# Kernel optimization log

Measured on AMD Instinct MI355X. Metric: run time of the kernel, lower is better.

## Reference

```python
import jax, jax.numpy as jnp
import numpy as np

H = 8          # head_num
NEG = -1e9     # mask fill value
LN_EPS = 1e-6


def setup_inputs() -> dict:
    key = jax.random.key(0)
    ks = jax.random.split(key, 12)
    B, S, D = 8, 1024, 512
    inp = {
        'q': jax.random.normal(ks[0], (B, S, D), jnp.float32),
        'k': jax.random.normal(ks[1], (B, S, D), jnp.float32),
        'v': jax.random.normal(ks[2], (B, S, D), jnp.float32),
        'query_mask': jax.random.randint(ks[3], (B, S), 0, 2, jnp.int32),
        'key_mask': jax.random.randint(ks[4], (B, S), 0, 2, jnp.int32),
        'Wq': jax.random.normal(ks[5], (D, D), jnp.float32) / np.sqrt(D),
        'bq': jax.random.normal(ks[6], (D,), jnp.float32) * 0.02,
        'Wk': jax.random.normal(ks[7], (D, D), jnp.float32) / np.sqrt(D),
        'bk': jax.random.normal(ks[8], (D,), jnp.float32) * 0.02,
        'Wv': jax.random.normal(ks[9], (D, D), jnp.float32) / np.sqrt(D),
        'bv': jax.random.normal(ks[10], (D,), jnp.float32) * 0.02,
        'gamma': jnp.ones((D,), jnp.float32),
        'beta': jnp.zeros((D,), jnp.float32),
    }
    return inp


def _to_batches(x):
    # [B,S,D] -> [B*H, S, D/H]  (batch-major head layout, as in torch code)
    B, S, D = x.shape
    return x.reshape(B, S, H, D // H).transpose(0, 2, 1, 3).reshape(B * H, S, D // H)


def _from_batches(x):
    BH, S, d = x.shape
    B = BH // H
    return x.reshape(B, H, S, d).transpose(0, 2, 1, 3).reshape(B, S, H * d)


def reference(q, k, v, query_mask, key_mask, Wq, bq, Wk, bk, Wv, bv, gamma, beta):
    # QKV linears + ReLU activation (activation=F.relu in original)
    _q = jax.nn.relu(q @ Wq.T + bq)
    _k = jax.nn.relu(k @ Wk.T + bk)
    _v = jax.nn.relu(v @ Wv.T + bv)
    _q, _k, _v = _to_batches(_q), _to_batches(_k), _to_batches(_v)  # [B*H,S,d]

    # masks tiled head-MAJOR (repeat(head_num,1) semantics): index = h*B + b
    km = jnp.tile(key_mask, (H, 1))[:, None, :]    # [B*H, 1, S_k]
    qm = jnp.tile(query_mask, (H, 1))[:, :, None]  # [B*H, S_q, 1]

    d = _q.shape[-1]
    scores = jnp.einsum('bqd,bkd->bqk', _q, _k) / jnp.sqrt(jnp.float32(d))
    scores = jnp.where(km == 0, NEG, scores)
    attn = jax.nn.softmax(scores, axis=-1)
    attn = attn * qm.astype(attn.dtype)            # multiplicative query mask
    # dropout: eval mode (rate applied only in training) -> identity
    y = jnp.einsum('bqk,bkd->bqd', attn, _v)
    y = _from_batches(y) + q                       # residual
    # LayerNorm over last dim
    mu = jnp.mean(y, axis=-1, keepdims=True)
    var = jnp.mean((y - mu) ** 2, axis=-1, keepdims=True)
    return gamma * (y - mu) / jnp.sqrt(var + LN_EPS) + beta
```

## Files before the change

kernel.cpp:

```cpp
#include <hip/hip_runtime.h>
#include <hip/hip_bf16.h>
#include <stdint.h>

constexpr int kB = 8, kH = 8, kS = 1024, kD = 512, kDH = 64;
constexpr float kNeg = -1e9f;
constexpr float kScaleLog2e = 0.125f * 1.4426950408889634f;

typedef __attribute__((ext_vector_type(8))) short bf16x8;
typedef __attribute__((ext_vector_type(4))) float f32x4;
typedef __attribute__((ext_vector_type(4))) unsigned short u16x4;

__device__ __forceinline__ unsigned short f2bf(float f) {
  union { float f; unsigned int u; } a; a.f = f;
  return (unsigned short)((a.u + 0x7FFFu + ((a.u >> 16) & 1u)) >> 16);
}

__device__ __forceinline__ unsigned int pk2bf(float lo, float hi) {
  union { __hip_bfloat162 h; unsigned int u; } cv;
  cv.h = __float22bfloat162_rn(make_float2(lo, hi));
  return cv.u;
}

__device__ __forceinline__ uint4 gload16(const void* p) {
  uint4 r;
  asm volatile("global_load_dwordx4 %0, %1, off" : "=v"(r) : "v"(p));
  return r;
}
__device__ __forceinline__ int gload4(const void* p) {
  int r;
  asm volatile("global_load_dword %0, %1, off" : "=v"(r) : "v"(p));
  return r;
}
__device__ __forceinline__ void wait_vmem() {
  asm volatile("s_waitcnt vmcnt(0)" ::: "memory");
  __builtin_amdgcn_sched_barrier(0);
}

__device__ __forceinline__ uint4 cvt4(uint4 a, uint4 b) {
  uint4 r;
  r.x = pk2bf(__uint_as_float(a.x), __uint_as_float(a.y));
  r.y = pk2bf(__uint_as_float(a.z), __uint_as_float(a.w));
  r.z = pk2bf(__uint_as_float(b.x), __uint_as_float(b.y));
  r.w = pk2bf(__uint_as_float(b.z), __uint_as_float(b.w));
  return r;
}

#if __has_builtin(__builtin_amdgcn_exp2f)
#define EXP2F(x) __builtin_amdgcn_exp2f(x)
#else
#define EXP2F(x) exp2f(x)
#endif

__global__ __launch_bounds__(256)
void wcvt_kernel(const float* __restrict__ wq, const float* __restrict__ wk,
                 const float* __restrict__ wv, unsigned short* __restrict__ wout)
{
  const int tid = blockIdx.x * 256 + threadIdx.x;
  const int z = tid >> 16;
  const int i = (tid & 65535) * 4;
  const float* W = (z == 0) ? wq : (z == 1) ? wk : wv;
  float4 v4 = *(const float4*)(W + i);
  u16x4 pk;
  pk[0] = f2bf(v4.x); pk[1] = f2bf(v4.y); pk[2] = f2bf(v4.z); pk[3] = f2bf(v4.w);
  *(u16x4*)(wout + (size_t)z * 262144 + i) = pk;
}

__global__ __launch_bounds__(256)
void qkv_gemm_kernel(const float* __restrict__ xq, const float* __restrict__ xk,
                     const float* __restrict__ xv,
                     const unsigned short* __restrict__ wbf,
                     const float* __restrict__ bq, const float* __restrict__ bk,
                     const float* __restrict__ bv,
                     unsigned short* __restrict__ wsout)
{
  __shared__ __align__(16) unsigned short As[128][72];
  __shared__ __align__(16) unsigned short Bs[128][72];

  const int bid = blockIdx.x;
  const int xcd = bid & 7;
  const int j = bid >> 3;
  const int x = j & 3;
  const int g = (j >> 2) * 8 + xcd;
  const int z = g >> 6;
  const int y = g & 63;

  const float* X    = (z == 0) ? xq : (z == 1) ? xk : xv;
  const unsigned short* Wb = wbf + (size_t)z * 262144;
  const float* bias = (z == 0) ? bq : (z == 1) ? bk : bv;
  unsigned short* out = wsout + (size_t)z * (kB * kS * kD);

  const int m0 = y * 128;
  const int n0 = x * 128;
  const int t = threadIdx.x;
  const int lane = t & 63;
  const int w = t >> 6;
  const int wr = w >> 1, wc = w & 1;
  const int l16 = lane & 15, lg = lane >> 4;

  const int row = t >> 3, c8 = (t & 7) * 8;
  const float* Xr = X + (size_t)(m0 + row) * kD + c8;
  const unsigned short* Wr = Wb + (size_t)(n0 + row) * kD + c8;

  f32x4 acc[4][4] = {};
  uint4 pa0, pa1, pa2, pa3, pa4, pa5, pa6, pa7;
  uint4 pb0, pb1, pb2, pb3;

  auto issue = [&](int kt) {
    pa0 = gload16(Xr + kt);            pa1 = gload16(Xr + kt + 4);
    pa2 = gload16(Xr + 32 * kD + kt);  pa3 = gload16(Xr + 32 * kD + kt + 4);
    pa4 = gload16(Xr + 64 * kD + kt);  pa5 = gload16(Xr + 64 * kD + kt + 4);
    pa6 = gload16(Xr + 96 * kD + kt);  pa7 = gload16(Xr + 96 * kD + kt + 4);
    pb0 = gload16(Wr + kt);
    pb1 = gload16(Wr + 32 * kD + kt);
    pb2 = gload16(Wr + 64 * kD + kt);
    pb3 = gload16(Wr + 96 * kD + kt);
  };
  auto lds_write = [&]() {
    wait_vmem();
    *(uint4*)&As[row][c8]      = cvt4(pa0, pa1);
    *(uint4*)&As[row + 32][c8] = cvt4(pa2, pa3);
    *(uint4*)&As[row + 64][c8] = cvt4(pa4, pa5);
    *(uint4*)&As[row + 96][c8] = cvt4(pa6, pa7);
    *(uint4*)&Bs[row][c8]      = pb0;
    *(uint4*)&Bs[row + 32][c8] = pb1;
    *(uint4*)&Bs[row + 64][c8] = pb2;
    *(uint4*)&Bs[row + 96][c8] = pb3;
  };
  auto mfma_phase = [&]() {
#pragma unroll
    for (int kk = 0; kk < 2; ++kk) {
      bf16x8 av[4], bv[4];
#pragma unroll
      for (int mf = 0; mf < 4; ++mf)
        av[mf] = *(const bf16x8*)&As[wr * 64 + mf * 16 + l16][kk * 32 + lg * 8];
#pragma unroll
      for (int nf = 0; nf < 4; ++nf)
        bv[nf] = *(const bf16x8*)&Bs[wc * 64 + nf * 16 + l16][kk * 32 + lg * 8];
#pragma unroll
      for (int nf = 0; nf < 4; ++nf)
#pragma unroll
        for (int mf = 0; mf < 4; ++mf)
          acc[mf][nf] = __builtin_amdgcn_mfma_f32_16x16x32_bf16(bv[nf], av[mf], acc[mf][nf], 0, 0, 0);
    }
  };

  issue(0);
  lds_write();
  __syncthreads();
#pragma unroll
  for (int i = 0; i < 8; ++i) {
    if (i < 7) issue((i + 1) * 64);
    mfma_phase();
    if (i < 7) {
      __syncthreads();
      lds_write();
      __syncthreads();
    }
  }

  if (z == 2) {
    const int mmbase = m0 + wr * 64;
    const int b_ = mmbase >> 10, sbase = mmbase & 1023;
#pragma unroll
    for (int nf = 0; nf < 4; ++nf) {
#pragma unroll
      for (int r = 0; r < 4; ++r) {
        const int n = n0 + wc * 64 + nf * 16 + lg * 4 + r;
        const float bval = bias[n];
        const int h = n >> 6, dd = n & 63;
        u16x4 pk;
#pragma unroll
        for (int mf = 0; mf < 4; ++mf) {
          float vv = acc[mf][nf][r] + bval;
          vv = vv > 0.f ? vv : 0.f;
          pk[mf] = f2bf(vv);
        }
        *(u16x4*)&out[((size_t)((b_ * kH + h) * kDH + dd)) * kS + sbase + l16 * 4] = pk;
      }
    }
  } else {
#pragma unroll
    for (int mf = 0; mf < 4; ++mf) {
      const int mm = m0 + wr * 64 + mf * 16 + l16;
      const int b_ = mm >> 10, s = mm & 1023;
#pragma unroll
      for (int nf = 0; nf < 4; ++nf) {
        const int nbase = n0 + wc * 64 + nf * 16 + lg * 4;
        const int h = nbase >> 6, dd = nbase & 63;
        u16x4 pk;
#pragma unroll
        for (int r = 0; r < 4; ++r) {
          float vv = acc[mf][nf][r] + bias[nbase + r];
          vv = vv > 0.f ? vv : 0.f;
          pk[r] = f2bf(vv);
        }
        *(u16x4*)&out[((size_t)(b_ * kH + h) * kS + s) * kDH + dd] = pk;
      }
    }
  }
}

__global__ __launch_bounds__(256)
void attn_kernel(const unsigned short* __restrict__ ws,
                 const int* __restrict__ key_mask,
                 float* __restrict__ y)
{
  __shared__ __align__(16) unsigned short Ks[2][64][72];
  __shared__ __align__(16) unsigned short Vts[2][64][72];
  __shared__ __align__(16) unsigned short Ps[4][16][72];
  __shared__ float kmadd[2][64];

  const unsigned short* Qw = ws;
  const unsigned short* Kw = ws + (size_t)1 * kB * kS * kD;
  const unsigned short* Vw = ws + (size_t)2 * kB * kS * kD;

  const int bid = blockIdx.x;
  const int xcd = bid & 7;
  const int j = bid >> 3;
  const int qx = j & 15;
  const int bh = (j >> 4) * 8 + xcd;

  const int q0 = qx * 64;
  const int t = threadIdx.x;
  const int w = t >> 6, lane = t & 63;
  const int l16 = lane & 15, lg = lane >> 4;
  const int b_ = bh / kH, h = bh % kH;

  const unsigned short* Qb = Qw + ((size_t)bh * kS + q0) * kDH;
  const unsigned short* Kb = Kw + (size_t)bh * kS * kDH;
  const unsigned short* Vb = Vw + (size_t)bh * kDH * kS;
  const int* km = key_mask + (bh % kB) * kS;

  const int srow = t >> 3, sc8 = (t & 7) * 8;
  const unsigned short* KbR0 = Kb + (size_t)srow * kDH + sc8;
  const unsigned short* KbR1 = Kb + (size_t)(srow + 32) * kDH + sc8;
  const unsigned short* VbR0 = Vb + (size_t)srow * kS + sc8;
  const unsigned short* VbR1 = Vb + (size_t)(srow + 32) * kS + sc8;

  bf16x8 aq[2];
#pragma unroll
  for (int kk = 0; kk < 2; ++kk)
    aq[kk] = *(const bf16x8*)(Qb + (size_t)(w * 16 + l16) * kDH + kk * 32 + lg * 8);

  bf16x8 vone;
#pragma unroll
  for (int jj = 0; jj < 8; ++jj) vone[jj] = (short)0x3F80;

  f32x4 o[4] = {};
  f32x4 lacc = {};

  uint4 ka0, ka1, va0, va1; int kmv = 0;

  auto issue = [&](int kv0) {
    ka0 = gload16(KbR0 + (size_t)kv0 * kDH);
    ka1 = gload16(KbR1 + (size_t)kv0 * kDH);
    va0 = gload16(VbR0 + kv0);
    va1 = gload16(VbR1 + kv0);
    if (t < 64) kmv = gload4(km + kv0 + t);
  };
  auto stage_write = [&](int buf) {
    wait_vmem();
    *(uint4*)&Ks[buf][srow][sc8]       = ka0;
    *(uint4*)&Ks[buf][srow + 32][sc8]  = ka1;
    *(uint4*)&Vts[buf][srow][sc8]      = va0;
    *(uint4*)&Vts[buf][srow + 32][sc8] = va1;
    if (t < 64) kmadd[buf][t] = kmv ? 0.f : kNeg;
  };
  auto compute = [&](int buf) {
    f32x4 sc[4] = {};
#pragma unroll
    for (int kk = 0; kk < 2; ++kk) {
#pragma unroll
      for (int nf = 0; nf < 4; ++nf) {
        bf16x8 bfr = *(const bf16x8*)&Ks[buf][nf * 16 + l16][kk * 32 + lg * 8];
        sc[nf] = __builtin_amdgcn_mfma_f32_16x16x32_bf16(aq[kk], bfr, sc[nf], 0, 0, 0);
      }
    }
    float madd[4];
#pragma unroll
    for (int nf = 0; nf < 4; ++nf) madd[nf] = kmadd[buf][nf * 16 + l16];
#pragma unroll
    for (int r = 0; r < 4; ++r) {
      const float p0 = EXP2F(fmaf(sc[0][r], kScaleLog2e, madd[0]));
      const float p1 = EXP2F(fmaf(sc[1][r], kScaleLog2e, madd[1]));
      const float p2 = EXP2F(fmaf(sc[2][r], kScaleLog2e, madd[2]));
      const float p3 = EXP2F(fmaf(sc[3][r], kScaleLog2e, madd[3]));
      const int prow = lg * 4 + r;
      uint2 pw;
      pw.x = __builtin_amdgcn_perm(__float_as_uint(p1), __float_as_uint(p0), 0x07060302u);
      pw.y = __builtin_amdgcn_perm(__float_as_uint(p3), __float_as_uint(p2), 0x07060302u);
      *(uint2*)&Ps[w][prow][l16 * 4] = pw;
    }
#pragma unroll
    for (int kk = 0; kk < 2; ++kk) {
      bf16x8 a = *(const bf16x8*)&Ps[w][l16][kk * 32 + lg * 8];
#pragma unroll
      for (int nd = 0; nd < 4; ++nd) {
        bf16x8 bfr = *(const bf16x8*)&Vts[buf][nd * 16 + l16][kk * 32 + lg * 8];
        o[nd] = __builtin_amdgcn_mfma_f32_16x16x32_bf16(a, bfr, o[nd], 0, 0, 0);
      }
      lacc = __builtin_amdgcn_mfma_f32_16x16x32_bf16(a, vone, lacc, 0, 0, 0);
    }
  };

  issue(0);
  stage_write(0);
  __syncthreads();
  for (int i = 0; i < 16; ++i) {
    if (i < 15) issue((i + 1) * 64);
    compute(i & 1);
    if (i < 15) stage_write((i + 1) & 1);
    __syncthreads();
  }

  float rinv[4];
#pragma unroll
  for (int r = 0; r < 4; ++r) rinv[r] = 1.f / lacc[r];
#pragma unroll
  for (int nd = 0; nd < 4; ++nd) {
#pragma unroll
    for (int r = 0; r < 4; ++r) {
      const int srowq = q0 + w * 16 + lg * 4 + r;
      y[((size_t)b_ * kS + srowq) * kD + h * kDH + nd * 16 + l16] = o[nd][r] * rinv[r];
    }
  }
}

__global__ __launch_bounds__(256)
void ln_kernel(const float* __restrict__ y, const float* __restrict__ q,
               const int* __restrict__ qmask,
               const float* __restrict__ gamma, const float* __restrict__ beta,
               float* __restrict__ out)
{
  const int w = threadIdx.x >> 6, lane = threadIdx.x & 63;
  const int row = blockIdx.x * 4 + w;
  const int b_ = row >> 10, s = row & 1023;
  const int d0 = lane * 8;
  const int h = d0 >> 6;

  const float* yp = y + (size_t)row * kD + d0;
  const float* qp = q + (size_t)row * kD + d0;
  const int qm = qmask[((b_ * kH + h) % kB) * kS + s];

  float4 y0 = *(const float4*)yp, y1 = *(const float4*)(yp + 4);
  float4 q0 = *(const float4*)qp, q1 = *(const float4*)(qp + 4);
  float vals[8] = { y0.x, y0.y, y0.z, y0.w, y1.x, y1.y, y1.z, y1.w };
  float qs[8]   = { q0.x, q0.y, q0.z, q0.w, q1.x, q1.y, q1.z, q1.w };

  float sum = 0.f, ss = 0.f;
#pragma unroll
  for (int j = 0; j < 8; ++j) {
    const float val = (qm ? vals[j] : 0.f) + qs[j];
    vals[j] = val; sum += val; ss += val * val;
  }
#pragma unroll
  for (int off = 1; off < 64; off <<= 1) {
    sum += __shfl_xor(sum, off);
    ss  += __shfl_xor(ss, off);
  }
  const float mu = sum * (1.f / kD);
  const float var = ss * (1.f / kD) - mu * mu;
  const float rstd = rsqrtf(var + 1e-6f);

  float4 g0 = *(const float4*)(gamma + d0), g1 = *(const float4*)(gamma + d0 + 4);
  float4 be0 = *(const float4*)(beta + d0), be1 = *(const float4*)(beta + d0 + 4);
  float gs[8] = { g0.x, g0.y, g0.z, g0.w, g1.x, g1.y, g1.z, g1.w };
  float bs[8] = { be0.x, be0.y, be0.z, be0.w, be1.x, be1.y, be1.z, be1.w };

  float4 o0, o1;
  o0.x = gs[0] * (vals[0] - mu) * rstd + bs[0];
  o0.y = gs[1] * (vals[1] - mu) * rstd + bs[1];
  o0.z = gs[2] * (vals[2] - mu) * rstd + bs[2];
  o0.w = gs[3] * (vals[3] - mu) * rstd + bs[3];
  o1.x = gs[4] * (vals[4] - mu) * rstd + bs[4];
  o1.y = gs[5] * (vals[5] - mu) * rstd + bs[5];
  o1.z = gs[6] * (vals[6] - mu) * rstd + bs[6];
  o1.w = gs[7] * (vals[7] - mu) * rstd + bs[7];
  *(float4*)(out + (size_t)row * kD + d0) = o0;
  *(float4*)(out + (size_t)row * kD + d0 + 4) = o1;
}

extern "C" void kernel_launch(void* const* d_in, const int* in_sizes, int n_in,
                              void* d_out, int out_size, void* d_ws, size_t ws_size,
                              hipStream_t stream) {
  const float* q  = (const float*)d_in[0];
  const float* k  = (const float*)d_in[1];
  const float* v  = (const float*)d_in[2];
  const int* qmask = (const int*)d_in[3];
  const int* kmask = (const int*)d_in[4];
  const float* Wq = (const float*)d_in[5];
  const float* bq = (const float*)d_in[6];
  const float* Wk = (const float*)d_in[7];
  const float* bk = (const float*)d_in[8];
  const float* Wv = (const float*)d_in[9];
  const float* bv = (const float*)d_in[10];
  const float* gamma = (const float*)d_in[11];
  const float* beta  = (const float*)d_in[12];
  float* out = (float*)d_out;
  unsigned short* wsqkv = (unsigned short*)d_ws;
  unsigned short* wbf = (unsigned short*)d_out;

  wcvt_kernel<<<768, 256, 0, stream>>>(Wq, Wk, Wv, wbf);
  qkv_gemm_kernel<<<768, 256, 0, stream>>>(
      q, k, v, wbf, bq, bk, bv, wsqkv);
  attn_kernel<<<1024, 256, 0, stream>>>(wsqkv, kmask, out);
  ln_kernel<<<2048, 256, 0, stream>>>(out, q, qmask, gamma, beta, out);
}
```

Measured before the change: 84.38 us.

## Double-buffer LDS in QKV GEMM and widen attention tile to 128 queries

The QKV GEMM moves from a single LDS buffer with two barriers per step to ping-pong LDS buffers. Two register prefetch sets keep loads in flight, gated by partial vmcnt waits. The attention kernel gives each wave 32 query rows instead of 16, so every K/V tile staged in LDS is reused across twice as many queries, and half as many blocks are launched. It also adopts the same two-deep prefetch with partial vmcnt waits. The cost is more registers per thread, which may lower occupancy, plus fewer attention blocks to fill the GPU.

Result: faster. 72.37 us (-14.2%).

```diff
diff --git a/kernel.cpp b/kernel.cpp
--- a/kernel.cpp
+++ b/kernel.cpp
@@ -31,10 +31,9 @@
   asm volatile("global_load_dword %0, %1, off" : "=v"(r) : "v"(p));
   return r;
 }
-__device__ __forceinline__ void wait_vmem() {
-  asm volatile("s_waitcnt vmcnt(0)" ::: "memory");
-  __builtin_amdgcn_sched_barrier(0);
-}
+#define WAIT_VMCNT(N) do { \
+  asm volatile("s_waitcnt vmcnt(" #N ")" ::: "memory"); \
+  __builtin_amdgcn_sched_barrier(0); } while (0)
 
 __device__ __forceinline__ uint4 cvt4(uint4 a, uint4 b) {
   uint4 r;
@@ -73,8 +72,8 @@
                      const float* __restrict__ bv,
                      unsigned short* __restrict__ wsout)
 {
-  __shared__ __align__(16) unsigned short As[128][72];
-  __shared__ __align__(16) unsigned short Bs[128][72];
+  __shared__ __align__(16) unsigned short As[2][128][72];
+  __shared__ __align__(16) unsigned short Bs[2][128][72];
 
   const int bid = blockIdx.x;
   const int xcd = bid & 7;
@@ -102,40 +101,55 @@
   const unsigned short* Wr = Wb + (size_t)(n0 + row) * kD + c8;
 
   f32x4 acc[4][4] = {};
-  uint4 pa0, pa1, pa2, pa3, pa4, pa5, pa6, pa7;
-  uint4 pb0, pb1, pb2, pb3;
-
-  auto issue = [&](int kt) {
+  uint4 pa0, pa1, pa2, pa3, pa4, pa5, pa6, pa7, pb0, pb1, pb2, pb3;
+  uint4 qa0, qa1, qa2, qa3, qa4, qa5, qa6, qa7, qb0, qb1, qb2, qb3;
+
+  auto issueP = [&](int kt) {
     pa0 = gload16(Xr + kt);            pa1 = gload16(Xr + kt + 4);
     pa2 = gload16(Xr + 32 * kD + kt);  pa3 = gload16(Xr + 32 * kD + kt + 4);
     pa4 = gload16(Xr + 64 * kD + kt);  pa5 = gload16(Xr + 64 * kD + kt + 4);
     pa6 = gload16(Xr + 96 * kD + kt);  pa7 = gload16(Xr + 96 * kD + kt + 4);
-    pb0 = gload16(Wr + kt);
-    pb1 = gload16(Wr + 32 * kD + kt);
-    pb2 = gload16(Wr + 64 * kD + kt);
-    pb3 = gload16(Wr + 96 * kD + kt);
-  };
-  auto lds_write = [&]() {
-    wait_vmem();
-    *(uint4*)&As[row][c8]      = cvt4(pa0, pa1);
-    *(uint4*)&As[row + 32][c8] = cvt4(pa2, pa3);
-    *(uint4*)&As[row + 64][c8] = cvt4(pa4, pa5);
-    *(uint4*)&As[row + 96][c8] = cvt4(pa6, pa7);
-    *(uint4*)&Bs[row][c8]      = pb0;
-    *(uint4*)&Bs[row + 32][c8] = pb1;
-    *(uint4*)&Bs[row + 64][c8] = pb2;
-    *(uint4*)&Bs[row + 96][c8] = pb3;
-  };
-  auto mfma_phase = [&]() {
+    pb0 = gload16(Wr + kt);            pb1 = gload16(Wr + 32 * kD + kt);
+    pb2 = gload16(Wr + 64 * kD + kt);  pb3 = gload16(Wr + 96 * kD + kt);
+  };
+  auto issueQ = [&](int kt) {
+    qa0 = gload16(Xr + kt);            qa1 = gload16(Xr + kt + 4);
+    qa2 = gload16(Xr + 32 * kD + kt);  qa3 = gload16(Xr + 32 * kD + kt + 4);
+    qa4 = gload16(Xr + 64 * kD + kt);  qa5 = gload16(Xr + 64 * kD + kt + 4);
+    qa6 = gload16(Xr + 96 * kD + kt);  qa7 = gload16(Xr + 96 * kD + kt + 4);
+    qb0 = gload16(Wr + kt);            qb1 = gload16(Wr + 32 * kD + kt);
+    qb2 = gload16(Wr + 64 * kD + kt);  qb3 = gload16(Wr + 96 * kD + kt);
+  };
+  auto writeP = [&]() {
+    *(uint4*)&As[0][row][c8]      = cvt4(pa0, pa1);
+    *(uint4*)&As[0][row + 32][c8] = cvt4(pa2, pa3);
+    *(uint4*)&As[0][row + 64][c8] = cvt4(pa4, pa5);
+    *(uint4*)&As[0][row + 96][c8] = cvt4(pa6, pa7);
+    *(uint4*)&Bs[0][row][c8]      = pb0;
+    *(uint4*)&Bs[0][row + 32][c8] = pb1;
+    *(uint4*)&Bs[0][row + 64][c8] = pb2;
+    *(uint4*)&Bs[0][row + 96][c8] = pb3;
+  };
+  auto writeQ = [&]() {
+    *(uint4*)&As[1][row][c8]      = cvt4(qa0, qa1);
+    *(uint4*)&As[1][row + 32][c8] = cvt4(qa2, qa3);
+    *(uint4*)&As[1][row + 64][c8] = cvt4(qa4, qa5);
+    *(uint4*)&As[1][row + 96][c8] = cvt4(qa6, qa7);
+    *(uint4*)&Bs[1][row][c8]      = qb0;
+    *(uint4*)&Bs[1][row + 32][c8] = qb1;
+    *(uint4*)&Bs[1][row + 64][c8] = qb2;
+    *(uint4*)&Bs[1][row + 96][c8] = qb3;
+  };
+  auto mfma_phase = [&](int buf) {
 #pragma unroll
     for (int kk = 0; kk < 2; ++kk) {
       bf16x8 av[4], bv[4];
 #pragma unroll
       for (int mf = 0; mf < 4; ++mf)
-        av[mf] = *(const bf16x8*)&As[wr * 64 + mf * 16 + l16][kk * 32 + lg * 8];
+        av[mf] = *(const bf16x8*)&As[buf][wr * 64 + mf * 16 + l16][kk * 32 + lg * 8];
 #pragma unroll
       for (int nf = 0; nf < 4; ++nf)
-        bv[nf] = *(const bf16x8*)&Bs[wc * 64 + nf * 16 + l16][kk * 32 + lg * 8];
+        bv[nf] = *(const bf16x8*)&Bs[buf][wc * 64 + nf * 16 + l16][kk * 32 + lg * 8];
 #pragma unroll
       for (int nf = 0; nf < 4; ++nf)
 #pragma unroll
@@ -144,19 +158,29 @@
     }
   };
 
-  issue(0);
-  lds_write();
+  issueP(0);
+  issueQ(64);
+#pragma unroll
+  for (int i = 0; i < 6; i += 2) {
+    WAIT_VMCNT(12);
+    writeP();
+    issueP((i + 2) * 64);
+    __syncthreads();
+    mfma_phase(0);
+    WAIT_VMCNT(12);
+    writeQ();
+    issueQ((i + 3) * 64);
+    __syncthreads();
+    mfma_phase(1);
+  }
+  WAIT_VMCNT(12);
+  writeP();
   __syncthreads();
-#pragma unroll
-  for (int i = 0; i < 8; ++i) {
-    if (i < 7) issue((i + 1) * 64);
-    mfma_phase();
-    if (i < 7) {
-      __syncthreads();
-      lds_write();
-      __syncthreads();
-    }
-  }
+  mfma_phase(0);
+  WAIT_VMCNT(0);
+  writeQ();
+  __syncthreads();
+  mfma_phase(1);
 
   if (z == 2) {
     const int mmbase = m0 + wr * 64;
@@ -207,7 +231,7 @@
 {
   __shared__ __align__(16) unsigned short Ks[2][64][72];
   __shared__ __align__(16) unsigned short Vts[2][64][72];
-  __shared__ __align__(16) unsigned short Ps[4][16][72];
+  __shared__ __align__(16) unsigned short Ps[4][32][72];
   __shared__ float kmadd[2][64];
 
   const unsigned short* Qw = ws;
@@ -217,10 +241,10 @@
   const int bid = blockIdx.x;
   const int xcd = bid & 7;
   const int j = bid >> 3;
-  const int qx = j & 15;
-  const int bh = (j >> 4) * 8 + xcd;
-
-  const int q0 = qx * 64;
+  const int qx = j & 7;
+  const int bh = (j >> 3) * 8 + xcd;
+
+  const int q0 = qx * 128;
   const int t = threadIdx.x;
   const int w = t >> 6, lane = t & 63;
   const int l16 = lane & 15, lg = lane >> 4;
@@ -237,91 +261,131 @@
   const unsigned short* VbR0 = Vb + (size_t)srow * kS + sc8;
   const unsigned short* VbR1 = Vb + (size_t)(srow + 32) * kS + sc8;
 
-  bf16x8 aq[2];
-#pragma unroll
-  for (int kk = 0; kk < 2; ++kk)
-    aq[kk] = *(const bf16x8*)(Qb + (size_t)(w * 16 + l16) * kDH + kk * 32 + lg * 8);
+  bf16x8 aq[2][2];
+#pragma unroll
+  for (int u = 0; u < 2; ++u)
+#pragma unroll
+    for (int kk = 0; kk < 2; ++kk)
+      aq[u][kk] = *(const bf16x8*)(Qb + (size_t)(w * 32 + u * 16 + l16) * kDH + kk * 32 + lg * 8);
 
   bf16x8 vone;
 #pragma unroll
   for (int jj = 0; jj < 8; ++jj) vone[jj] = (short)0x3F80;
 
-  f32x4 o[4] = {};
-  f32x4 lacc = {};
-
-  uint4 ka0, ka1, va0, va1; int kmv = 0;
-
-  auto issue = [&](int kv0) {
+  f32x4 o[2][4] = {};
+  f32x4 lacc[2] = {};
+
+  uint4 ka0, ka1, va0, va1; int kma;
+  uint4 kb0, kb1, vb0, vb1; int kmb;
+
+  auto issueA = [&](int kv0) {
     ka0 = gload16(KbR0 + (size_t)kv0 * kDH);
     ka1 = gload16(KbR1 + (size_t)kv0 * kDH);
     va0 = gload16(VbR0 + kv0);
     va1 = gload16(VbR1 + kv0);
-    if (t < 64) kmv = gload4(km + kv0 + t);
-  };
-  auto stage_write = [&](int buf) {
-    wait_vmem();
-    *(uint4*)&Ks[buf][srow][sc8]       = ka0;
-    *(uint4*)&Ks[buf][srow + 32][sc8]  = ka1;
-    *(uint4*)&Vts[buf][srow][sc8]      = va0;
-    *(uint4*)&Vts[buf][srow + 32][sc8] = va1;
-    if (t < 64) kmadd[buf][t] = kmv ? 0.f : kNeg;
+    kma = gload4(km + kv0 + (t & 63));
+  };
+  auto issueB = [&](int kv0) {
+    kb0 = gload16(KbR0 + (size_t)kv0 * kDH);
+    kb1 = gload16(KbR1 + (size_t)kv0 * kDH);
+    vb0 = gload16(VbR0 + kv0);
+    vb1 = gload16(VbR1 + kv0);
+    kmb = gload4(km + kv0 + (t & 63));
+  };
+  auto writeA = [&]() {
+    *(uint4*)&Ks[0][srow][sc8]       = ka0;
+    *(uint4*)&Ks[0][srow + 32][sc8]  = ka1;
+    *(uint4*)&Vts[0][srow][sc8]      = va0;
+    *(uint4*)&Vts[0][srow + 32][sc8] = va1;
+    if (t < 64) kmadd[0][t] = kma ? 0.f : kNeg;
+  };
+  auto writeB = [&]() {
+    *(uint4*)&Ks[1][srow][sc8]       = kb0;
+    *(uint4*)&Ks[1][srow + 32][sc8]  = kb1;
+    *(uint4*)&Vts[1][srow][sc8]      = vb0;
+    *(uint4*)&Vts[1][srow + 32][sc8] = vb1;
+    if (t < 64) kmadd[1][t] = kmb ? 0.f : kNeg;
   };
   auto compute = [&](int buf) {
-    f32x4 sc[4] = {};
+    f32x4 sc[2][4] = {};
 #pragma unroll
     for (int kk = 0; kk < 2; ++kk) {
 #pragma unroll
       for (int nf = 0; nf < 4; ++nf) {
         bf16x8 bfr = *(const bf16x8*)&Ks[buf][nf * 16 + l16][kk * 32 + lg * 8];
-        sc[nf] = __builtin_amdgcn_mfma_f32_16x16x32_bf16(aq[kk], bfr, sc[nf], 0, 0, 0);
+#pragma unroll
+        for (int u = 0; u < 2; ++u)
+          sc[u][nf] = __builtin_amdgcn_mfma_f32_16x16x32_bf16(aq[u][kk], bfr, sc[u][nf], 0, 0, 0);
       }
     }
     float madd[4];
 #pragma unroll
     for (int nf = 0; nf < 4; ++nf) madd[nf] = kmadd[buf][nf * 16 + l16];
 #pragma unroll
-    for (int r = 0; r < 4; ++r) {
-      const float p0 = EXP2F(fmaf(sc[0][r], kScaleLog2e, madd[0]));
-      const float p1 = EXP2F(fmaf(sc[1][r], kScaleLog2e, madd[1]));
-      const float p2 = EXP2F(fmaf(sc[2][r], kScaleLog2e, madd[2]));
-      const float p3 = EXP2F(fmaf(sc[3][r], kScaleLog2e, madd[3]));
-      const int prow = lg * 4 + r;
-      uint2 pw;
-      pw.x = __builtin_amdgcn_perm(__float_as_uint(p1), __float_as_uint(p0), 0x07060302u);
-      pw.y = __builtin_amdgcn_perm(__float_as_uint(p3), __float_as_uint(p2), 0x07060302u);
-      *(uint2*)&Ps[w][prow][l16 * 4] = pw;
+    for (int u = 0; u < 2; ++u) {
+#pragma unroll
+      for (int r = 0; r < 4; ++r) {
+        const float p0 = EXP2F(fmaf(sc[u][0][r], kScaleLog2e, madd[0]));
+        const float p1 = EXP2F(fmaf(sc[u][1][r], kScaleLog2e, madd[1]));
+        const float p2 = EXP2F(fmaf(sc[u][2][r], kScaleLog2e, madd[2]));
+        const float p3 = EXP2F(fmaf(sc[u][3][r], kScaleLog2e, madd[3]));
+        const int prow = u * 16 + lg * 4 + r;
+        uint2 pw;
+        pw.x = __builtin_amdgcn_perm(__float_as_uint(p1), __float_as_uint(p0), 0x07060302u);
+        pw.y = __builtin_amdgcn_perm(__float_as_uint(p3), __float_as_uint(p2), 0x07060302u);
+        *(uint2*)&Ps[w][prow][l16 * 4] = pw;
+      }
     }
 #pragma unroll
     for (int kk = 0; kk < 2; ++kk) {
-      bf16x8 a = *(const bf16x8*)&Ps[w][l16][kk * 32 + lg * 8];
+      bf16x8 a0 = *(const bf16x8*)&Ps[w][l16][kk * 32 + lg * 8];
+      bf16x8 a1 = *(const bf16x8*)&Ps[w][16 + l16][kk * 32 + lg * 8];
 #pragma unroll
       for (int nd = 0; nd < 4; ++nd) {
         bf16x8 bfr = *(const bf16x8*)&Vts[buf][nd * 16 + l16][kk * 32 + lg * 8];
-        o[nd] = __builtin_amdgcn_mfma_f32_16x16x32_bf16(a, bfr, o[nd], 0, 0, 0);
-      }
-      lacc = __builtin_amdgcn_mfma_f32_16x16x32_bf16(a, vone, lacc, 0, 0, 0);
-    }
-  };
-
-  issue(0);
-  stage_write(0);
+        o[0][nd] = __builtin_amdgcn_mfma_f32_16x16x32_bf16(a0, bfr, o[0][nd], 0, 0, 0);
+        o[1][nd] = __builtin_amdgcn_mfma_f32_16x16x32_bf16(a1, bfr, o[1][nd], 0, 0, 0);
+      }
+      lacc[0] = __builtin_amdgcn_mfma_f32_16x16x32_bf16(a0, vone, lacc[0], 0, 0, 0);
+      lacc[1] = __builtin_amdgcn_mfma_f32_16x16x32_bf16(a1, vone, lacc[1], 0, 0, 0);
+    }
+  };
+
+  issueA(0);
+  issueB(64);
+  for (int i = 0; i < 14; i += 2) {
+    WAIT_VMCNT(5);
+    writeA();
+    issueA((i + 2) * 64);
+    __syncthreads();
+    compute(0);
+    WAIT_VMCNT(5);
+    writeB();
+    issueB((i + 3) * 64);
+    __syncthreads();
+    compute(1);
+  }
+  WAIT_VMCNT(5);
+  writeA();
   __syncthreads();
-  for (int i = 0; i < 16; ++i) {
-    if (i < 15) issue((i + 1) * 64);
-    compute(i & 1);
-    if (i < 15) stage_write((i + 1) & 1);
-    __syncthreads();
-  }
-
-  float rinv[4];
-#pragma unroll
-  for (int r = 0; r < 4; ++r) rinv[r] = 1.f / lacc[r];
-#pragma unroll
-  for (int nd = 0; nd < 4; ++nd) {
-#pragma unroll
-    for (int r = 0; r < 4; ++r) {
-      const int srowq = q0 + w * 16 + lg * 4 + r;
-      y[((size_t)b_ * kS + srowq) * kD + h * kDH + nd * 16 + l16] = o[nd][r] * rinv[r];
+  compute(0);
+  WAIT_VMCNT(0);
+  writeB();
+  __syncthreads();
+  compute(1);
+
+#pragma unroll
+  for (int u = 0; u < 2; ++u) {
+    float rinv[4];
+#pragma unroll
+    for (int r = 0; r < 4; ++r) rinv[r] = 1.f / lacc[u][r];
+#pragma unroll
+    for (int nd = 0; nd < 4; ++nd) {
+#pragma unroll
+      for (int r = 0; r < 4; ++r) {
+        const int srowq = q0 + w * 32 + u * 16 + lg * 4 + r;
+        y[((size_t)b_ * kS + srowq) * kD + h * kDH + nd * 16 + l16] = o[u][nd][r] * rinv[r];
+      }
     }
   }
 }
@@ -403,6 +467,6 @@
   wcvt_kernel<<<768, 256, 0, stream>>>(Wq, Wk, Wv, wbf);
   qkv_gemm_kernel<<<768, 256, 0, stream>>>(
       q, k, v, wbf, bq, bk, bv, wsqkv);
-  attn_kernel<<<1024, 256, 0, stream>>>(wsqkv, kmask, out);
+  attn_kernel<<<512, 256, 0, stream>>>(wsqkv, kmask, out);
   ln_kernel<<<2048, 256, 0, stream>>>(out, q, qmask, gamma, beta, out);
 }
```
